# Kernel tuning notes

Hardware: AMD Instinct MI355X
Metric: run time of the kernel (lower is better)

The kernel has to match this reference:

```python
import jax, jax.numpy as jnp
import numpy as np

N_NODES = 50000
N_EDGES = 800000
D_IN = 512
D_OUT = 256


def setup_inputs() -> dict:
    key = jax.random.key(0)
    k1, k2, k3 = jax.random.split(key, 3)
    x = jax.random.normal(k1, (N_NODES, D_IN), dtype=jnp.float32)
    edge_index = jax.random.randint(k2, (2, N_EDGES), 0, N_NODES, dtype=jnp.int64)
    # Glorot-style init for the GCN weight, zero bias (PyG defaults)
    W = jax.random.normal(k3, (D_IN, D_OUT), dtype=jnp.float32) * (1.0 / np.sqrt(D_IN))
    b = jnp.zeros((D_OUT,), dtype=jnp.float32)
    return {"x": x, "edge_index": edge_index, "W": W, "b": b}


def reference(x, edge_index, W, b):
    N = x.shape[0]
    # 1) dense linear transform (the compute-heavy GEMM)
    xw = x @ W  # [N, d_out]

    # 2) add self-loops (PyG GCNConv default)
    loop = jnp.arange(N, dtype=edge_index.dtype)
    row = jnp.concatenate([edge_index[0], loop])  # sources
    col = jnp.concatenate([edge_index[1], loop])  # targets

    # 3) symmetric normalization deg^{-1/2} on targets (in-degree incl. self-loops)
    deg = jax.ops.segment_sum(jnp.ones_like(col, dtype=xw.dtype), col, num_segments=N)
    dinv = jnp.where(deg > 0, jax.lax.rsqrt(deg), 0.0)
    norm = dinv[row] * dinv[col]  # [E+N]

    # 4) gather source features, scale, scatter-add to targets
    msgs = xw[row] * norm[:, None]  # [E+N, d_out]
    agg = jax.ops.segment_sum(msgs, col, num_segments=N)  # [N, d_out]

    # 5) bias + ReLU (dropout is identity in eval mode)
    return jax.nn.relu(agg + b)
```

## Files before the change

kernel.cpp:

```cpp
#include <hip/hip_runtime.h>
#include <hip/hip_bf16.h>

#define N_NODES 50000
#define N_EDGES 800000
#define D_IN    512
#define D_OUT   256
#define NBLK_SCAN ((N_NODES + 1023) / 1024)
#define GEMM_NWG (((N_NODES + 127) / 128) * 2)
#define GEMM_Q   (GEMM_NWG / 8)
#define GEMM_R   (GEMM_NWG % 8)
#define GATH_CHUNKS ((N_NODES + 63) / 64)

typedef short s8v  __attribute__((ext_vector_type(8)));
typedef float f32x4 __attribute__((ext_vector_type(4)));

__device__ __forceinline__ unsigned short bf16b(float f) {
    __hip_bfloat16 h = __float2bfloat16(f);
    return *reinterpret_cast<unsigned short*>(&h);
}
__device__ __forceinline__ float bflo(unsigned u) { return __uint_as_float(u << 16); }
__device__ __forceinline__ float bfhi(unsigned u) { return __uint_as_float(u & 0xffff0000u); }

#define GLD16(gp, lp)                                                           \
    __builtin_amdgcn_global_load_lds(                                           \
        (const __attribute__((address_space(1))) unsigned int*)(const void*)(gp),\
        (__attribute__((address_space(3))) unsigned int*)(void*)(lp), 16, 0, 0)

__device__ __forceinline__ int wave_incl_scan(int v, int lane) {
    #pragma unroll
    for (int d = 1; d < 64; d <<= 1) {
        int u = __shfl_up(v, d, 64);
        if (lane >= d) v += u;
    }
    return v;
}

__global__ void k_wt(const float* __restrict__ W, unsigned short* __restrict__ Wt,
                     int* __restrict__ cnt4) {
    int k = blockIdx.x;
    int n = threadIdx.x;
    Wt[(size_t)n * D_IN + k] = bf16b(W[(size_t)k * D_OUT + n]);
    int t = (blockIdx.x * 256 + threadIdx.x) * 2;
    if (t < 4 * N_NODES) {
        cnt4[t] = 0;
        if (t + 1 < 4 * N_NODES) cnt4[t + 1] = 0;
    }
}


__global__ void k_count(const int* __restrict__ col, int* __restrict__ cnt4) {
    int i = (blockIdx.x * 256 + threadIdx.x) * 2;
    if (i < N_EDGES) {
        int2 c = *(const int2*)&col[i];
        atomicAdd(&cnt4[(i & 3) * N_NODES + c.x], 1);
        atomicAdd(&cnt4[((i + 1) & 3) * N_NODES + c.y], 1);
    }
}

__launch_bounds__(256)
__global__ void k_scan1(const int* __restrict__ cnt4, int* __restrict__ bsum) {
    const int t = threadIdx.x, b = blockIdx.x;
    const int idx = b * 1024 + t * 4;
    int s = 0;
    if (idx < N_NODES) {
        #pragma unroll
        for (int q = 0; q < 4; ++q) {
            int4 v = *(const int4*)&cnt4[q * N_NODES + idx];
            s += (v.x + v.y) + (v.z + v.w);
        }
    }
    #pragma unroll
    for (int d = 1; d < 64; d <<= 1) s += __shfl_xor(s, d, 64);
    __shared__ int ws[4];
    if ((t & 63) == 0) ws[t >> 6] = s;
    __syncthreads();
    if (t == 0) bsum[b] = ws[0] + ws[1] + ws[2] + ws[3];
}

__launch_bounds__(256)
__global__ void k_scan3(const int* __restrict__ cnt4, const int* __restrict__ bsum,
                        int* __restrict__ row_ptr, float* __restrict__ dinv,
                        int* __restrict__ cursor4) {
    const int t = threadIdx.x, b = blockIdx.x;
    const int lane = t & 63, wv = t >> 6;
    const int idx = b * 1024 + t * 4;
    int4 vq[4];
    int4 tot = make_int4(0, 0, 0, 0);
    if (idx < N_NODES) {
        #pragma unroll
        for (int q = 0; q < 4; ++q) {
            vq[q] = *(const int4*)&cnt4[q * N_NODES + idx];
            tot.x += vq[q].x; tot.y += vq[q].y;
            tot.z += vq[q].z; tot.w += vq[q].w;
        }
    } else {
        #pragma unroll
        for (int q = 0; q < 4; ++q) vq[q] = make_int4(0, 0, 0, 0);
    }
    int s = (tot.x + tot.y) + (tot.z + tot.w);
    int isc = wave_incl_scan(s, lane);
    __shared__ int wsum[4];
    __shared__ int s_boff;
    if (lane == 63) wsum[wv] = isc;
    if (t < 64) {
        int u = (t < b) ? bsum[t] : 0;
        #pragma unroll
        for (int d = 1; d < 64; d <<= 1) u += __shfl_xor(u, d, 64);
        if (t == 0) s_boff = u;
    }
    __syncthreads();
    int off = s_boff;
    #pragma unroll
    for (int i = 0; i < 4; ++i)
        if (i < wv) off += wsum[i];
    int p0 = off + isc - s;
    int p1 = p0 + tot.x;
    int p2 = p1 + tot.y;
    int p3 = p2 + tot.z;
    if (idx < N_NODES) {
        row_ptr[idx + 0] = p0; dinv[idx + 0] = rsqrtf(1.f + (float)tot.x);
        row_ptr[idx + 1] = p1; dinv[idx + 1] = rsqrtf(1.f + (float)tot.y);
        row_ptr[idx + 2] = p2; dinv[idx + 2] = rsqrtf(1.f + (float)tot.z);
        row_ptr[idx + 3] = p3; dinv[idx + 3] = rsqrtf(1.f + (float)tot.w);
        int4 run = make_int4(p0, p1, p2, p3);
        #pragma unroll
        for (int q = 0; q < 4; ++q) {
            *(int4*)&cursor4[q * N_NODES + idx] = run;
            run.x += vq[q].x; run.y += vq[q].y;
            run.z += vq[q].z; run.w += vq[q].w;
        }
    }
    if (b == 0 && t == 0) row_ptr[N_NODES] = N_EDGES;
}

__global__ void k_fill(const int* __restrict__ row, const int* __restrict__ col,
                       int* __restrict__ cursor4, int* __restrict__ csr_src) {
    int i = (blockIdx.x * 256 + threadIdx.x) * 2;
    if (i < N_EDGES) {
        int2 c = *(const int2*)&col[i];
        int2 r = *(const int2*)&row[i];
        int p0 = atomicAdd(&cursor4[(i & 3) * N_NODES + c.x], 1);
        csr_src[p0] = r.x;
        int p1 = atomicAdd(&cursor4[((i + 1) & 3) * N_NODES + c.y], 1);
        csr_src[p1] = r.y;
    }
}

__launch_bounds__(256)
__global__ void k_gemm(const float* __restrict__ A,
                       const unsigned short* __restrict__ Wt,
                       const float* __restrict__ dinv,
                       unsigned short* __restrict__ yb)
{
    __shared__ __align__(16) float          As[2 * 128 * 32];
    __shared__ __align__(16) unsigned short Bs[2 * 128 * 32];

    int orig = blockIdx.x;
    int xcd = orig % 8, pos = orig / 8;
    int wg = (xcd < GEMM_R) ? xcd * (GEMM_Q + 1) + pos
                            : GEMM_R * (GEMM_Q + 1) + (xcd - GEMM_R) * GEMM_Q + pos;
    const int nt = wg & 1;
    const int mt = wg >> 1;
    const int m0 = mt * 128;
    const int n0 = nt * 128;

    const int t  = threadIdx.x;
    const int w  = t >> 6;
    const int l  = t & 63;
    const int wm = (w >> 1) * 64;
    const int wn = (w & 1) * 64;
    const int lr = l & 15;
    const int lk = l >> 4;

    size_t aoff[4];
    #pragma unroll
    for (int i = 0; i < 4; ++i) {
        int r = m0 + w * 32 + i * 8 + (l >> 3);
        if (r >= N_NODES) r = 0;
        aoff[i] = (size_t)r * D_IN + ((l & 7) ^ (l >> 3)) * 4;
    }
    size_t boff[2];
    #pragma unroll
    for (int i = 0; i < 2; ++i) {
        int r = n0 + w * 32 + i * 16 + (l >> 2);
        boff[i] = (size_t)r * D_IN + ((l & 3) ^ ((l >> 3) & 3)) * 8;
    }

    f32x4 acc[4][4] = {};

    #define STAGE(buf, kk)                                                       \
        do {                                                                     \
            char* ab = (char*)As + (buf) * 16384 + w * 4096;                     \
            char* bb = (char*)Bs + (buf) * 8192  + w * 2048;                     \
            _Pragma("unroll")                                                    \
            for (int i = 0; i < 4; ++i) GLD16(&A[aoff[i] + (kk)], ab + i * 1024);\
            _Pragma("unroll")                                                    \
            for (int i = 0; i < 2; ++i) GLD16(&Wt[boff[i] + (kk)], bb + i * 1024);\
        } while (0)

    #define COMPUTE(buf)                                                         \
        do {                                                                     \
            const char* abase = (const char*)As + (buf) * 16384;                 \
            const char* bbase = (const char*)Bs + (buf) * 8192;                  \
            s8v af[4], bfr[4];                                                   \
            _Pragma("unroll")                                                    \
            for (int f = 0; f < 4; ++f) {                                        \
                int row = wm + f * 16 + lr;                   \
                int s0  = (2 * lk) ^ (lr & 7);                                   \
                const char* pr = abase + row * 128;                              \
                float4 x0 = *(const float4*)(pr + s0 * 16);                      \
                float4 x1 = *(const float4*)(pr + (s0 ^ 1) * 16);                \
                union { s8v v; unsigned short h[8]; } u;                         \
                u.h[0] = bf16b(x0.x); u.h[1] = bf16b(x0.y);                      \
                u.h[2] = bf16b(x0.z); u.h[3] = bf16b(x0.w);                      \
                u.h[4] = bf16b(x1.x); u.h[5] = bf16b(x1.y);                      \
                u.h[6] = bf16b(x1.z); u.h[7] = bf16b(x1.w);                      \
                af[f] = u.v;                                                     \
            }                                                                    \
            _Pragma("unroll")                                                    \
            for (int f = 0; f < 4; ++f) {                                        \
                int row = wn + f * 16 + lr;         \
                int s   = lk ^ ((lr >> 1) & 3);                                  \
                bfr[f] = *(const s8v*)(bbase + row * 64 + s * 16);               \
            }                                                                    \
            _Pragma("unroll")                                                    \
            for (int fm = 0; fm < 4; ++fm)                                       \
                _Pragma("unroll")                                                \
                for (int fn = 0; fn < 4; ++fn)                                   \
                    acc[fm][fn] = __builtin_amdgcn_mfma_f32_16x16x32_bf16(       \
                        af[fm], bfr[fn], acc[fm][fn], 0, 0, 0);                  \
        } while (0)

    STAGE(0, 0);
    STAGE(1, 32);
    asm volatile("s_waitcnt vmcnt(6)" ::: "memory");
    __builtin_amdgcn_s_barrier();

    #pragma unroll 1
    for (int tk = 0; tk < 14; ++tk) {
        COMPUTE(tk & 1);
        __builtin_amdgcn_s_barrier();
        STAGE(tk & 1, (tk + 2) * 32);
        asm volatile("s_waitcnt vmcnt(6)" ::: "memory");
        __builtin_amdgcn_s_barrier();
    }
    COMPUTE(0);
    __builtin_amdgcn_s_barrier();
    asm volatile("s_waitcnt vmcnt(0)" ::: "memory");
    __builtin_amdgcn_s_barrier();
    COMPUTE(1);

    #undef STAGE
    #undef COMPUTE

    #pragma unroll
    for (int fm = 0; fm < 4; ++fm) {
        #pragma unroll
        for (int j = 0; j < 4; ++j) {
            int row = m0 + wm + fm * 16 + lk * 4 + j;
            if (row < N_NODES) {
                float s = dinv[row];
                #pragma unroll
                for (int fn = 0; fn < 4; ++fn) {
                    int col = n0 + wn + fn * 16 + lr;
                    size_t off = (size_t)(col >> 5) * (N_NODES * 32)
                               + (size_t)row * 32 + (col & 31);
                    yb[off] = bf16b(acc[fm][fn][j] * s);
                }
            }
        }
    }
}

__device__ __forceinline__ void add8(float* acc, uint4 q) {
    unsigned x;
    x = q.x; acc[0] += bflo(x); acc[1] += bfhi(x);
    x = q.y; acc[2] += bflo(x); acc[3] += bfhi(x);
    x = q.z; acc[4] += bflo(x); acc[5] += bfhi(x);
    x = q.w; acc[6] += bflo(x); acc[7] += bfhi(x);
}

__launch_bounds__(256)
__global__ void k_gather(const int* __restrict__ row_ptr, const int* __restrict__ csr_src,
                         const unsigned short* __restrict__ yb,
                         const float* __restrict__ dinv,
                         const float* __restrict__ bias, float* __restrict__ out)
{
    const int s     = blockIdx.x & 7;
    const int chunk = blockIdx.x >> 3;
    const int g     = threadIdx.x >> 2;
    const int cs    = threadIdx.x & 3;
    const int c     = chunk * 64 + g;
    if (c >= N_NODES) return;

    const uint4* t4 = (const uint4*)(yb + (size_t)s * N_NODES * 32);

    float acc[8] = {0.f,0.f,0.f,0.f,0.f,0.f,0.f,0.f};

    const int e0 = row_ptr[c];
    const int e1 = row_ptr[c + 1];
    for (int i = e0; i < e1; i += 4) {
        int idx[4];
        #pragma unroll
        for (int j = 0; j < 4; ++j) {
            int p = i + j;
            idx[j] = csr_src[p < e1 ? p : e1 - 1];
        }
        uint4 v[4];
        #pragma unroll
        for (int j = 0; j < 4; ++j) v[j] = t4[(size_t)idx[j] * 4 + cs];
        #pragma unroll
        for (int j = 0; j < 4; ++j)
            if (i + j < e1) add8(acc, v[j]);
    }

    add8(acc, t4[(size_t)c * 4 + cs]);

    const float sc = dinv[c];
    const int colb = s * 32 + cs * 8;
    float4 b0 = *(const float4*)&bias[colb];
    float4 b1 = *(const float4*)&bias[colb + 4];
    float4 o0, o1;
    o0.x = fmaxf(fmaf(acc[0], sc, b0.x), 0.f);
    o0.y = fmaxf(fmaf(acc[1], sc, b0.y), 0.f);
    o0.z = fmaxf(fmaf(acc[2], sc, b0.z), 0.f);
    o0.w = fmaxf(fmaf(acc[3], sc, b0.w), 0.f);
    o1.x = fmaxf(fmaf(acc[4], sc, b1.x), 0.f);
    o1.y = fmaxf(fmaf(acc[5], sc, b1.y), 0.f);
    o1.z = fmaxf(fmaf(acc[6], sc, b1.z), 0.f);
    o1.w = fmaxf(fmaf(acc[7], sc, b1.w), 0.f);
    float* dst = &out[(size_t)c * D_OUT + colb];
    *(float4*)dst       = o0;
    *(float4*)(dst + 4) = o1;
}

extern "C" void kernel_launch(void* const* d_in, const int* in_sizes, int n_in,
                              void* d_out, int out_size, void* d_ws, size_t ws_size,
                              hipStream_t stream) {
    const float* x   = (const float*)d_in[0];
    const int*   ei  = (const int*)d_in[1];
    const float* W   = (const float*)d_in[2];
    const float* b   = (const float*)d_in[3];
    float*       out = (float*)d_out;

    const int* row = ei;
    const int* col = ei + N_EDGES;

    char* p = (char*)d_ws;
    unsigned short* yb = (unsigned short*)p;  p += (size_t)N_NODES * D_OUT * 2;
    unsigned short* Wt = (unsigned short*)p;  p += (size_t)D_OUT * D_IN * 2;
    int*   csr_src = (int*)p;                 p += (size_t)N_EDGES * 4;
    int*   cnt4    = (int*)p;                 p += (size_t)4 * N_NODES * 4;
    int*   row_ptr = (int*)p;                 p += (size_t)(N_NODES + 4) * 4;
    int*   cursor4 = (int*)p;                 p += (size_t)4 * N_NODES * 4;
    float* dinv    = (float*)p;               p += (size_t)N_NODES * 4;
    int*   bsum    = (int*)p;                 p += (size_t)NBLK_SCAN * 4;

    k_wt   <<<D_IN, D_OUT, 0, stream>>>(W, Wt, cnt4);
    k_count<<<(N_EDGES / 2 + 255) / 256, 256, 0, stream>>>(col, cnt4);
    k_scan1<<<NBLK_SCAN, 256, 0, stream>>>(cnt4, bsum);
    k_scan3<<<NBLK_SCAN, 256, 0, stream>>>(cnt4, bsum, row_ptr, dinv, cursor4);
    k_fill <<<(N_EDGES / 2 + 255) / 256, 256, 0, stream>>>(row, col, cursor4, csr_src);

    k_gemm<<<GEMM_NWG, 256, 0, stream>>>(x, Wt, dinv, yb);

    k_gather<<<GATH_CHUNKS * 8, 256, 0, stream>>>(row_ptr, csr_src, yb, dinv, b, out);
}
```

Baseline: 193.1 us.

## Replace direct-to-LDS double buffering with register-staged single-buffer GEMM pipeline

The GEMM main loop drops the global_load_lds double-buffered LDS scheme. It now prefetches the next K tile into registers, writes them to a single LDS buffer after compute, and publishes with an lgkmcnt wait and a barrier. LDS use is halved and launch bounds request two blocks per CU, aiming for higher occupancy. The cost is extra VGPRs for the staging registers, an explicit ds_write pass, and two barriers per iteration on a single buffer, which can serialize compute and LDS writes.

```diff
diff --git a/kernel.cpp b/kernel.cpp
--- a/kernel.cpp
+++ b/kernel.cpp
@@ -20,11 +20,6 @@
 }
 __device__ __forceinline__ float bflo(unsigned u) { return __uint_as_float(u << 16); }
 __device__ __forceinline__ float bfhi(unsigned u) { return __uint_as_float(u & 0xffff0000u); }
-
-#define GLD16(gp, lp)                                                           \
-    __builtin_amdgcn_global_load_lds(                                           \
-        (const __attribute__((address_space(1))) unsigned int*)(const void*)(gp),\
-        (__attribute__((address_space(3))) unsigned int*)(void*)(lp), 16, 0, 0)
 
 __device__ __forceinline__ int wave_incl_scan(int v, int lane) {
     #pragma unroll
@@ -146,14 +141,14 @@
     }
 }
 
-__launch_bounds__(256)
+__launch_bounds__(256, 2)
 __global__ void k_gemm(const float* __restrict__ A,
                        const unsigned short* __restrict__ Wt,
                        const float* __restrict__ dinv,
                        unsigned short* __restrict__ yb)
 {
-    __shared__ __align__(16) float          As[2 * 128 * 32];
-    __shared__ __align__(16) unsigned short Bs[2 * 128 * 32];
+    __shared__ __align__(16) float          As[128 * 32];
+    __shared__ __align__(16) unsigned short Bs[128 * 32];
 
     int orig = blockIdx.x;
     int xcd = orig % 8, pos = orig / 8;
@@ -172,42 +167,63 @@
     const int lr = l & 15;
     const int lk = l >> 4;
 
-    size_t aoff[4];
+    const float* agp[4];
+    unsigned     awb[4];
     #pragma unroll
     for (int i = 0; i < 4; ++i) {
-        int r = m0 + w * 32 + i * 8 + (l >> 3);
-        if (r >= N_NODES) r = 0;
-        aoff[i] = (size_t)r * D_IN + ((l & 7) ^ (l >> 3)) * 4;
-    }
-    size_t boff[2];
+        int rl = i * 32 + (t >> 3);
+        int rg = m0 + rl;
+        if (rg >= N_NODES) rg = 0;
+        agp[i] = A + (size_t)rg * D_IN + (t & 7) * 4;
+        awb[i] = rl * 128 + (((t & 7) ^ ((t >> 3) & 7)) << 4);
+    }
+    const unsigned short* bgp[2];
+    unsigned              bwb[2];
     #pragma unroll
     for (int i = 0; i < 2; ++i) {
-        int r = n0 + w * 32 + i * 16 + (l >> 2);
-        boff[i] = (size_t)r * D_IN + ((l & 3) ^ ((l >> 3) & 3)) * 8;
-    }
-
-    f32x4 acc[4][4] = {};
-
-    #define STAGE(buf, kk)                                                       \
+        int rl = i * 64 + (t >> 2);
+        bgp[i] = Wt + (size_t)(n0 + rl) * D_IN + (t & 3) * 8;
+        bwb[i] = rl * 64 + (((t & 3) ^ ((t >> 3) & 3)) << 4);
+    }
+
+    float4 ar[4];
+    uint4  br[2];
+
+    #define LOADR(kk)                                                \
+        do {                                                         \
+            _Pragma("unroll")                                        \
+            for (int i = 0; i < 4; ++i)                              \
+                ar[i] = *(const float4*)(agp[i] + (kk));             \
+            _Pragma("unroll")                                        \
+            for (int i = 0; i < 2; ++i)                              \
+                br[i] = *(const uint4*)(bgp[i] + (kk));              \
+        } while (0)
+
+    #define DSW()                                                    \
+        do {                                                         \
+            _Pragma("unroll")                                        \
+            for (int i = 0; i < 4; ++i)                              \
+                *(float4*)((char*)As + awb[i]) = ar[i];              \
+            _Pragma("unroll")                                        \
+            for (int i = 0; i < 2; ++i)                              \
+                *(uint4*)((char*)Bs + bwb[i]) = br[i];               \
+        } while (0)
+
+    #define PUBLISH()                                                \
+        do {                                                         \
+            asm volatile("s_waitcnt lgkmcnt(0)" ::: "memory");       \
+            __builtin_amdgcn_sched_barrier(0);                       \
+            __builtin_amdgcn_s_barrier();                            \
+        } while (0)
+
+    #define COMPUTE()                                                            \
         do {                                                                     \
-            char* ab = (char*)As + (buf) * 16384 + w * 4096;                     \
-            char* bb = (char*)Bs + (buf) * 8192  + w * 2048;                     \
-            _Pragma("unroll")                                                    \
-            for (int i = 0; i < 4; ++i) GLD16(&A[aoff[i] + (kk)], ab + i * 1024);\
-            _Pragma("unroll")                                                    \
-            for (int i = 0; i < 2; ++i) GLD16(&Wt[boff[i] + (kk)], bb + i * 1024);\
-        } while (0)
-
-    #define COMPUTE(buf)                                                         \
-        do {                                                                     \
-            const char* abase = (const char*)As + (buf) * 16384;                 \
-            const char* bbase = (const char*)Bs + (buf) * 8192;                  \
             s8v af[4], bfr[4];                                                   \
             _Pragma("unroll")                                                    \
             for (int f = 0; f < 4; ++f) {                                        \
                 int row = wm + f * 16 + lr;                   \
                 int s0  = (2 * lk) ^ (lr & 7);                                   \
-                const char* pr = abase + row * 128;                              \
+                const char* pr = (const char*)As + row * 128;                    \
                 float4 x0 = *(const float4*)(pr + s0 * 16);                      \
                 float4 x1 = *(const float4*)(pr + (s0 ^ 1) * 16);                \
                 union { s8v v; unsigned short h[8]; } u;                         \
@@ -221,7 +237,7 @@
             for (int f = 0; f < 4; ++f) {                                        \
                 int row = wn + f * 16 + lr;         \
                 int s   = lk ^ ((lr >> 1) & 3);                                  \
-                bfr[f] = *(const s8v*)(bbase + row * 64 + s * 16);               \
+                bfr[f] = *(const s8v*)((const char*)Bs + row * 64 + s * 16);     \
             }                                                                    \
             _Pragma("unroll")                                                    \
             for (int fm = 0; fm < 4; ++fm)                                       \
@@ -231,26 +247,26 @@
                         af[fm], bfr[fn], acc[fm][fn], 0, 0, 0);                  \
         } while (0)
 
-    STAGE(0, 0);
-    STAGE(1, 32);
-    asm volatile("s_waitcnt vmcnt(6)" ::: "memory");
-    __builtin_amdgcn_s_barrier();
+    f32x4 acc[4][4] = {};
+
+    LOADR(0);
+    DSW();
+    LOADR(32);
+    PUBLISH();
 
     #pragma unroll 1
-    for (int tk = 0; tk < 14; ++tk) {
-        COMPUTE(tk & 1);
+    for (int tk = 0; tk < 15; ++tk) {
+        COMPUTE();
         __builtin_amdgcn_s_barrier();
-        STAGE(tk & 1, (tk + 2) * 32);
-        asm volatile("s_waitcnt vmcnt(6)" ::: "memory");
-        __builtin_amdgcn_s_barrier();
-    }
-    COMPUTE(0);
-    __builtin_amdgcn_s_barrier();
-    asm volatile("s_waitcnt vmcnt(0)" ::: "memory");
-    __builtin_amdgcn_s_barrier();
-    COMPUTE(1);
-
-    #undef STAGE
+        DSW();
+        if (tk < 14) LOADR((tk + 2) * 32);
+        PUBLISH();
+    }
+    COMPUTE();
+
+    #undef LOADR
+    #undef DSW
+    #undef PUBLISH
     #undef COMPUTE
 
     #pragma unroll
```

New measurement: 263.4 us. 1.36x slower.
